# Kernel tuning notes

Measured on AMD Instinct MI355X. Metric: run time of the kernel, lower is better.

The kernel has to match this reference:

```python
import jax, jax.numpy as jnp
import numpy as np

S, B, D = 2048, 2, 1024
H, DH = 16, 64
DFF = 4096
E, K = 4, 2
SCALE = 1.0 / (DH ** 0.5)


def _ln(x, g, b, eps):
    m = jnp.mean(x, axis=-1, keepdims=True)
    v = jnp.mean((x - m) ** 2, axis=-1, keepdims=True)
    return (x - m) * jax.lax.rsqrt(v + eps) * g + b


def setup_inputs() -> dict:
    key = jax.random.key(0)
    ks = jax.random.split(key, 12)
    s = lambda k, shape, fan: jax.random.normal(k, shape, jnp.float32) * (fan ** -0.5)
    return {
        "hidden_states": jax.random.normal(ks[0], (S, B, D), jnp.float32),
        "ln_in_g": jnp.ones((D,), jnp.float32), "ln_in_b": jnp.zeros((D,), jnp.float32),
        "Wq": s(ks[1], (D, H * DH), D),
        "Wkv": s(ks[2], (D, 2 * H * DH), D),
        "Wo": s(ks[3], (H * DH, D), H * DH),
        "ln_attn_g": jnp.ones((D,), jnp.float32), "ln_attn_b": jnp.zeros((D,), jnp.float32),
        "ln_post_g": jnp.ones((D,), jnp.float32), "ln_post_b": jnp.zeros((D,), jnp.float32),
        "Wg": s(ks[4], (D, E), D),
        "W1": s(ks[5], (E, D, DFF), D), "b1": jnp.zeros((E, DFF), jnp.float32),
        "W2": s(ks[6], (E, DFF, D), DFF), "b2": jnp.zeros((E, D), jnp.float32),
    }


def reference(hidden_states, ln_in_g, ln_in_b, Wq, Wkv, Wo, ln_attn_g, ln_attn_b,
              ln_post_g, ln_post_b, Wg, W1, b1, W2, b2):
    # --- input layernorm (eps=1e-6) ---
    h = _ln(hidden_states, ln_in_g, ln_in_b, 1e-6)  # [S,B,D]

    # --- MultiHeadAttn2 (post-lnorm, no mask, no mems) ---
    q = (h @ Wq).reshape(S, B, H, DH)
    k, v = jnp.split((h @ Wkv).reshape(S, B, H, 2 * DH), 2, axis=-1)
    score = jnp.einsum('ibnd,jbnd->ijbn', q, k) * SCALE      # [S,S,B,H]
    prob = jax.nn.softmax(score, axis=1)
    attn_vec = jnp.einsum('ijbn,jbnd->ibnd', prob, v).reshape(S, B, H * DH)
    attn_out = attn_vec @ Wo
    attention_output = _ln(h + attn_out, ln_attn_g, ln_attn_b, 1e-5)

    # --- residual + post-attention layernorm (eps=1e-6) ---
    layernorm_input = hidden_states + attention_output
    x = _ln(layernorm_input, ln_post_g, ln_post_b, 1e-6)

    # --- top-k MoE (E=4, k=2, no token dropping) ---
    xt = x.reshape(-1, D)                                     # [T,D]
    probs = jax.nn.softmax(xt @ Wg, axis=-1)                  # [T,E]
    topv, topi = jax.lax.top_k(probs, K)                      # [T,K]
    gates = topv / jnp.sum(topv, axis=-1, keepdims=True)
    cw = jnp.zeros_like(probs)
    for kk in range(K):  # small fixed K
        cw = cw + gates[:, kk:kk + 1] * jax.nn.one_hot(topi[:, kk], E, dtype=probs.dtype)
    hmid = jax.nn.gelu(jnp.einsum('td,edf->tef', xt, W1) + b1, approximate=False)
    y = jnp.einsum('tef,efd->ted', hmid, W2) + b2             # [T,E,D]
    moe_out = jnp.einsum('te,ted->td', cw, y).reshape(S, B, D)

    # load-balancing aux loss: E * sum(mean_probs * top1_fraction)
    me = jnp.mean(probs, axis=0)
    ce = jnp.mean(jax.nn.one_hot(topi[:, 0], E, dtype=probs.dtype), axis=0)
    moe_loss = E * jnp.sum(me * ce)

    output = layernorm_input + moe_out
    return output, moe_loss
```

## Files before the change

### kernel.cpp

```cpp
#include <hip/hip_runtime.h>
#include <cmath>

#define S_   2048
#define B_   2
#define D_   1024
#define H_   16
#define DH_  64
#define DFF_ 4096
#define E_   4
#define T_   4096
#define SCALE_ 0.125f

typedef __attribute__((ext_vector_type(8))) short short8;
typedef __attribute__((ext_vector_type(4))) float f32x4;
typedef __attribute__((ext_vector_type(4))) unsigned short u16x4;
typedef __attribute__((ext_vector_type(4))) unsigned int u32x4;

static __device__ __forceinline__ unsigned short f2bf(float f) {
  union { float f; unsigned int u; } v; v.f = f;
  unsigned int r = v.u + 0x7FFFu + ((v.u >> 16) & 1u);
  return (unsigned short)(r >> 16);
}

static __device__ __forceinline__ float bf2f(unsigned short u) {
  union { unsigned int u; float f; } v; v.u = (unsigned int)u << 16;
  return v.f;
}

static __device__ __forceinline__ f32x4 mfma16(short8 a, short8 b, f32x4 c) {
  return __builtin_amdgcn_mfma_f32_16x16x32_bf16(a, b, c, 0, 0, 0);
}

static __device__ __forceinline__ void gll16(const unsigned short* g, unsigned short* l) {
  __builtin_amdgcn_global_load_lds(
      (const __attribute__((address_space(1))) void*)g,
      (__attribute__((address_space(3))) void*)l, 16, 0, 0);
}

static __device__ __forceinline__ float gelu_f(float vv) {
  float u = 0.7978845608f * (vv + 0.044715f * vv * vv * vv);
  u = fminf(fmaxf(u, -9.0f), 9.0f);
  float e2 = __expf(2.0f * u);
  return vv * e2 * (1.0f / (e2 + 1.0f));
}

__global__ void transpose_cvt(const float* __restrict__ in, unsigned short* __restrict__ out,
                              int R, int C) {
  __shared__ float t[64][33];
  size_t boff = (size_t)blockIdx.z * R * C;
  in += boff; out += boff;
  int c0 = blockIdx.x * 32, r0 = blockIdx.y * 64;
  for (int i = threadIdx.y; i < 64; i += 8)
    t[i][threadIdx.x] = in[(size_t)(r0 + i) * C + c0 + threadIdx.x];
  __syncthreads();
  for (int i = threadIdx.y; i < 32; i += 8) {
    float v0 = t[2 * threadIdx.x][i], v1 = t[2 * threadIdx.x + 1][i];
    unsigned int pk = (unsigned int)f2bf(v0) | ((unsigned int)f2bf(v1) << 16);
    *(unsigned int*)(&out[(size_t)(c0 + i) * R + r0 + 2 * threadIdx.x]) = pk;
  }
}

__global__ void transpose_cvt_split(const float* __restrict__ in,
    unsigned short* __restrict__ outh, unsigned short* __restrict__ outl, int R, int C) {
  __shared__ float t[64][33];
  int c0 = blockIdx.x * 32, r0 = blockIdx.y * 64;
  for (int i = threadIdx.y; i < 64; i += 8)
    t[i][threadIdx.x] = in[(size_t)(r0 + i) * C + c0 + threadIdx.x];
  __syncthreads();
  for (int i = threadIdx.y; i < 32; i += 8) {
    float v0 = t[2 * threadIdx.x][i], v1 = t[2 * threadIdx.x + 1][i];
    unsigned short h0 = f2bf(v0), h1 = f2bf(v1);
    unsigned int hp = (unsigned int)h0 | ((unsigned int)h1 << 16);
    unsigned int lp = (unsigned int)f2bf(v0 - bf2f(h0)) |
                      ((unsigned int)f2bf(v1 - bf2f(h1)) << 16);
    size_t o = (size_t)(c0 + i) * R + r0 + 2 * threadIdx.x;
    *(unsigned int*)(&outh[o]) = hp;
    *(unsigned int*)(&outl[o]) = lp;
  }
}

__global__ __launch_bounds__(256) void v_transpose(
    const unsigned short* __restrict__ kvh, const unsigned short* __restrict__ kvl,
    unsigned short* __restrict__ vTh, unsigned short* __restrict__ vTl) {
  __shared__ unsigned short th[64][72], tl[64][72];
  int j0 = blockIdx.x * 64;
  int bh = blockIdx.y;
  int b = bh & 1, n = bh >> 1;
  int tid = threadIdx.x;
  int jr = tid >> 3, dc = (tid & 7) * 8;
  for (int it = 0; it < 2; ++it) {
    int jj = it * 32 + jr;
    size_t src = ((size_t)((j0 + jj) * 2 + b)) * 2048 + n * 128 + 64 + dc;
    *(short8*)(&th[jj][dc]) = *(const short8*)(kvh + src);
    *(short8*)(&tl[jj][dc]) = *(const short8*)(kvl + src);
  }
  __syncthreads();
  int dr = tid >> 3, jc = (tid & 7) * 8;
  for (int it = 0; it < 2; ++it) {
    int d = it * 32 + dr;
    short8 oh, ol;
    for (int u = 0; u < 8; ++u) { oh[u] = th[jc + u][d]; ol[u] = tl[jc + u][d]; }
    size_t dst = ((size_t)((b * 16 + n) * 64 + d)) * 2048 + j0 + jc;
    *(short8*)(vTh + dst) = oh;
    *(short8*)(vTl + dst) = ol;
  }
}

static __device__ __forceinline__ void block_reduce2(float& s, float& s2, float* sh) {
  __syncthreads();
  for (int off = 32; off; off >>= 1) { s += __shfl_down(s, off); s2 += __shfl_down(s2, off); }
  int w = threadIdx.x >> 6;
  if ((threadIdx.x & 63) == 0) { sh[w * 2] = s; sh[w * 2 + 1] = s2; }
  __syncthreads();
  s = sh[0] + sh[2] + sh[4] + sh[6];
  s2 = sh[1] + sh[3] + sh[5] + sh[7];
}

__global__ __launch_bounds__(256) void ln_in_kernel(const float* __restrict__ hid,
    const float* __restrict__ g, const float* __restrict__ b,
    float* __restrict__ h, unsigned short* __restrict__ hbh, unsigned short* __restrict__ hbl) {
  __shared__ float sh[8];
  int t = blockIdx.x, tid = threadIdx.x;
  size_t ro = (size_t)t * D_;
  f32x4 v = ((const f32x4*)(hid + ro))[tid];
  float s = v[0] + v[1] + v[2] + v[3];
  float s2 = v[0]*v[0] + v[1]*v[1] + v[2]*v[2] + v[3]*v[3];
  block_reduce2(s, s2, sh);
  float mean = s * (1.0f / D_);
  float var = s2 * (1.0f / D_) - mean * mean;
  float rstd = rsqrtf(var + 1e-6f);
  f32x4 gv = ((const f32x4*)g)[tid], bv = ((const f32x4*)b)[tid];
  f32x4 y; u16x4 yh, yl;
  for (int c = 0; c < 4; ++c) {
    float z = (v[c] - mean) * rstd * gv[c] + bv[c];
    y[c] = z; yh[c] = f2bf(z); yl[c] = f2bf(z - bf2f(yh[c]));
  }
  ((f32x4*)(h + ro))[tid] = y;
  ((u16x4*)(hbh + ro))[tid] = yh;
  ((u16x4*)(hbl + ro))[tid] = yl;
}

__global__ __launch_bounds__(256) void ln_fused_kernel(
    const float* __restrict__ hid, const float* __restrict__ h, const float* __restrict__ ao,
    const float* __restrict__ ga, const float* __restrict__ ba,
    const float* __restrict__ gp, const float* __restrict__ bp,
    float* __restrict__ out, float* __restrict__ x, unsigned short* __restrict__ xb) {
  __shared__ float sh[8];
  int t = blockIdx.x, tid = threadIdx.x;
  size_t ro = (size_t)t * D_;
  f32x4 hv = ((const f32x4*)(h + ro))[tid];
  f32x4 av = ((const f32x4*)(ao + ro))[tid];
  f32x4 a = hv + av;
  float s = a[0] + a[1] + a[2] + a[3];
  float s2 = a[0]*a[0] + a[1]*a[1] + a[2]*a[2] + a[3]*a[3];
  block_reduce2(s, s2, sh);
  float mean = s * (1.0f / D_);
  float var = s2 * (1.0f / D_) - mean * mean;
  float rstd = rsqrtf(var + 1e-5f);
  f32x4 lg = ((const f32x4*)ga)[tid], lb = ((const f32x4*)ba)[tid];
  f32x4 hidv = ((const f32x4*)(hid + ro))[tid];
  f32x4 li;
  for (int c = 0; c < 4; ++c) li[c] = hidv[c] + (a[c] - mean) * rstd * lg[c] + lb[c];
  ((f32x4*)(out + ro))[tid] = li;
  float s3 = li[0] + li[1] + li[2] + li[3];
  float s4 = li[0]*li[0] + li[1]*li[1] + li[2]*li[2] + li[3]*li[3];
  block_reduce2(s3, s4, sh);
  float mean2 = s3 * (1.0f / D_);
  float var2 = s4 * (1.0f / D_) - mean2 * mean2;
  float rstd2 = rsqrtf(var2 + 1e-6f);
  f32x4 g2 = ((const f32x4*)gp)[tid], b2v = ((const f32x4*)bp)[tid];
  f32x4 xv; u16x4 xbv;
  for (int c = 0; c < 4; ++c) { float z = (li[c] - mean2) * rstd2 * g2[c] + b2v[c]; xv[c] = z; xbv[c] = f2bf(z); }
  ((f32x4*)(x + ro))[tid] = xv;
  ((u16x4*)(xb + ro))[tid] = xbv;
}

__global__ __launch_bounds__(256) void qkv_gemm(
    const unsigned short* __restrict__ Ah, const unsigned short* __restrict__ Al,
    const unsigned short* __restrict__ WqTh, const unsigned short* __restrict__ WqTl,
    const unsigned short* __restrict__ WkvTh, const unsigned short* __restrict__ WkvTl,
    unsigned short* __restrict__ qh, unsigned short* __restrict__ ql,
    unsigned short* __restrict__ kvh, unsigned short* __restrict__ kvl) {
  const int K = 1024;
  int m0 = blockIdx.y * 128, n0g = blockIdx.x * 128;
  const unsigned short *Bh, *Bl;
  unsigned short *Ch, *Cl;
  int NC, n0;
  float cscale;
  if (n0g < 1024) { Bh = WqTh; Bl = WqTl; Ch = qh; Cl = ql; NC = 1024; n0 = n0g; cscale = SCALE_; }
  else { Bh = WkvTh; Bl = WkvTl; Ch = kvh; Cl = kvl; NC = 2048; n0 = n0g - 1024; cscale = 1.0f; }
  __shared__ unsigned short pool2[32768];
  unsigned short* buf[2] = { pool2, pool2 + 16384 };
  int tid = threadIdx.x;
  int lane = tid & 63, w = tid >> 6;
  int quad = lane >> 4, l15 = lane & 15;
  int wm = (w >> 1) * 64, wn = (w & 1) * 64;
  f32x4 acc[4][4];
  for (int i = 0; i < 4; ++i) for (int j = 0; j < 4; ++j) acc[i][j] = 0;
  int rs0 = w * 32 + (lane >> 2), rs1 = rs0 + 16;
  int sw = ((lane & 3) ^ ((lane >> 3) & 3)) * 8;
  const unsigned short* gah0 = Ah + (size_t)(m0 + rs0) * K + sw;
  const unsigned short* gah1 = Ah + (size_t)(m0 + rs1) * K + sw;
  const unsigned short* gal0 = Al + (size_t)(m0 + rs0) * K + sw;
  const unsigned short* gal1 = Al + (size_t)(m0 + rs1) * K + sw;
  const unsigned short* gbh0 = Bh + (size_t)(n0 + rs0) * K + sw;
  const unsigned short* gbh1 = Bh + (size_t)(n0 + rs1) * K + sw;
  const unsigned short* gbl0 = Bl + (size_t)(n0 + rs0) * K + sw;
  const unsigned short* gbl1 = Bl + (size_t)(n0 + rs1) * K + sw;
  int so0 = (w * 2 + 0) * 512, so1 = (w * 2 + 1) * 512;
  int sq = (l15 >> 1) & 3;
  auto stage = [&](unsigned short* bb, int k) {
    gll16(gah0 + k, bb + so0);         gll16(gah1 + k, bb + so1);
    gll16(gal0 + k, bb + 4096 + so0);  gll16(gal1 + k, bb + 4096 + so1);
    gll16(gbh0 + k, bb + 8192 + so0);  gll16(gbh1 + k, bb + 8192 + so1);
    gll16(gbl0 + k, bb + 12288 + so0); gll16(gbl1 + k, bb + 12288 + so1);
  };
  auto compute = [&](const unsigned short* bb) {
    short8 afh[4], afl[4], bfh[4], bfl[4];
    for (int i = 0; i < 4; ++i) {
      int o = (wm + i * 16 + l15) * 32 + ((quad ^ sq) * 8);
      afh[i] = *(const short8*)(&bb[o]);
      afl[i] = *(const short8*)(&bb[4096 + o]);
    }
    for (int j = 0; j < 4; ++j) {
      int o = (wn + j * 16 + l15) * 32 + ((quad ^ sq) * 8);
      bfh[j] = *(const short8*)(&bb[8192 + o]);
      bfl[j] = *(const short8*)(&bb[12288 + o]);
    }
    for (int i = 0; i < 4; ++i)
      for (int j = 0; j < 4; ++j) {
        f32x4 a = acc[i][j];
        a = mfma16(afh[i], bfl[j], a);
        a = mfma16(afl[i], bfh[j], a);
        a = mfma16(afh[i], bfh[j], a);
        acc[i][j] = a;
      }
  };
  stage(buf[0], 0);
  __syncthreads();
  for (int k0 = 0; k0 < K; k0 += 64) {
    stage(buf[1], k0 + 32);
    compute(buf[0]);
    __syncthreads();
    if (k0 + 64 < K) stage(buf[0], k0 + 64);
    compute(buf[1]);
    __syncthreads();
  }
  unsigned short* eph = &pool2[w * 1152];
  unsigned short* epl = &pool2[4608 + w * 1152];
  int row16 = lane >> 3, chunk = lane & 7;
  for (int i = 0; i < 4; ++i) {
    for (int j = 0; j < 4; ++j) {
      f32x4 a = acc[i][j];
      int lo = j * 16 + l15;
      for (int r = 0; r < 4; ++r) {
        float av = a[r] * cscale;
        unsigned short hb = f2bf(av);
        eph[(quad * 4 + r) * 72 + lo] = hb;
        epl[(quad * 4 + r) * 72 + lo] = f2bf(av - bf2f(hb));
      }
    }
    for (int it = 0; it < 2; ++it) {
      int rr = it * 8 + row16;
      size_t go = (size_t)(m0 + wm + i * 16 + rr) * NC + n0 + wn + chunk * 8;
      *(u32x4*)(&Ch[go]) = *(const u32x4*)(&eph[rr * 72 + chunk * 8]);
      *(u32x4*)(&Cl[go]) = *(const u32x4*)(&epl[rr * 72 + chunk * 8]);
    }
    __syncthreads();
  }
}

template<int MT>
__global__ __launch_bounds__(256) void gemm3f(
    const unsigned short* __restrict__ Ah, const unsigned short* __restrict__ Al,
    const unsigned short* __restrict__ Bh, const unsigned short* __restrict__ Bl,
    float* __restrict__ Cf, int N, int K) {
  int m0 = blockIdx.y * MT, n0 = blockIdx.x * 128;
  __shared__ unsigned short pool3[MT * 64 + 8192];
  unsigned short* Ash = pool3;
  unsigned short* Asl = pool3 + MT * 32;
  unsigned short* Bsh = pool3 + MT * 64;
  unsigned short* Bsl = pool3 + MT * 64 + 4096;
  int tid = threadIdx.x;
  int lane = tid & 63, w = tid >> 6;
  int quad = lane >> 4, l15 = lane & 15;
  int wm = (w >> 1) * (MT / 2), wn = (w & 1) * 64;
  constexpr int MI = MT / 32;
  f32x4 acc[MI][4];
  for (int i = 0; i < MI; ++i) for (int j = 0; j < 4; ++j) acc[i][j] = 0;
  constexpr int AI = MT / 64;
  int cofs = (lane & 3) * 8;
  const unsigned short* gah[AI]; const unsigned short* gal[AI];
  unsigned short *lAh[AI], *lAl[AI];
  for (int is = 0; is < AI; ++is) {
    int rs = w * (MT / 4) + is * 16 + (lane >> 2);
    gah[is] = Ah + (size_t)(m0 + rs) * K + cofs;
    gal[is] = Al + (size_t)(m0 + rs) * K + cofs;
    lAh[is] = &Ash[(w * AI + is) * 512];
    lAl[is] = &Asl[(w * AI + is) * 512];
  }
  int rsB0 = w * 32 + (lane >> 2), rsB1 = rsB0 + 16;
  const unsigned short* gbh0 = Bh + (size_t)(n0 + rsB0) * K + cofs;
  const unsigned short* gbh1 = Bh + (size_t)(n0 + rsB1) * K + cofs;
  const unsigned short* gbl0 = Bl + (size_t)(n0 + rsB0) * K + cofs;
  const unsigned short* gbl1 = Bl + (size_t)(n0 + rsB1) * K + cofs;
  unsigned short* lB0 = &Bsh[(w * 2 + 0) * 512];
  unsigned short* lB1 = &Bsh[(w * 2 + 1) * 512];
  unsigned short* lBl0 = &Bsl[(w * 2 + 0) * 512];
  unsigned short* lBl1 = &Bsl[(w * 2 + 1) * 512];
  for (int k0 = 0; k0 < K; k0 += 32) {
    __syncthreads();
    for (int is = 0; is < AI; ++is) { gll16(gah[is] + k0, lAh[is]); gll16(gal[is] + k0, lAl[is]); }
    gll16(gbh0 + k0, lB0); gll16(gbh1 + k0, lB1);
    gll16(gbl0 + k0, lBl0); gll16(gbl1 + k0, lBl1);
    __syncthreads();
    short8 afh[MI], afl[MI], bfh[4], bfl[4];
    for (int i = 0; i < MI; ++i) {
      int o = (wm + i * 16 + l15) * 32 + quad * 8;
      afh[i] = *(const short8*)(&Ash[o]);
      afl[i] = *(const short8*)(&Asl[o]);
    }
    for (int j = 0; j < 4; ++j) {
      int o = (wn + j * 16 + l15) * 32 + quad * 8;
      bfh[j] = *(const short8*)(&Bsh[o]);
      bfl[j] = *(const short8*)(&Bsl[o]);
    }
    for (int i = 0; i < MI; ++i)
      for (int j = 0; j < 4; ++j) {
        f32x4 a = acc[i][j];
        a = mfma16(afh[i], bfl[j], a);
        a = mfma16(afl[i], bfh[j], a);
        a = mfma16(afh[i], bfh[j], a);
        acc[i][j] = a;
      }
  }
  __syncthreads();
  float* epf = (float*)(pool3 + w * 2176);
  for (int i = 0; i < MI; ++i) {
    for (int j = 0; j < 4; ++j) {
      f32x4 a = acc[i][j];
      for (int r = 0; r < 4; ++r) epf[(quad * 4 + r) * 68 + j * 16 + l15] = a[r];
    }
    for (int it = 0; it < 4; ++it) {
      int rr = (lane >> 4) + it * 4;
      int ch = lane & 15;
      *(f32x4*)(&Cf[(size_t)(m0 + wm + i * 16 + rr) * N + n0 + wn + ch * 4]) =
          *(const f32x4*)(&epf[rr * 68 + ch * 4]);
    }
    __syncthreads();
  }
}

__global__ __launch_bounds__(256) void moe_up(
    const unsigned short* __restrict__ A, const unsigned short* __restrict__ W1T,
    unsigned short* __restrict__ hmid, int N, int K,
    const int* __restrict__ cnt, const int* __restrict__ offs,
    const int* __restrict__ list, const float* __restrict__ b1) {
  int e = blockIdx.y >> 5, mt = blockIdx.y & 31;
  int M = cnt[e];
  int m0 = mt * 128, n0 = blockIdx.x * 128;
  if (M == 0 || m0 >= M) return;
  const unsigned short* Bt = W1T + (size_t)e * DFF_ * D_;
  const int* liste = list + e * T_;
  const float* bias = b1 + (size_t)e * DFF_;
  size_t obase = (size_t)offs[e];
  __shared__ unsigned short pool[16384];
  unsigned short* As0 = pool;
  unsigned short* Bs0 = pool + 4096;
  unsigned short* As1 = pool + 8192;
  unsigned short* Bs1 = pool + 12288;
  int tid = threadIdx.x;
  int lane = tid & 63, w = tid >> 6;
  int quad = lane >> 4, l15 = lane & 15;
  int wm = (w >> 1) * 64, wn = (w & 1) * 64;
  f32x4 acc[4][4];
  for (int i = 0; i < 4; ++i) for (int j = 0; j < 4; ++j) acc[i][j] = 0;
  int rs0 = w * 32 + (lane >> 2), rs1 = rs0 + 16;
  int sw = ((lane & 3) ^ ((lane >> 3) & 3)) * 8;
  const unsigned short* ga0 = A + (size_t)liste[min(m0 + rs0, M - 1)] * K + sw;
  const unsigned short* ga1 = A + (size_t)liste[min(m0 + rs1, M - 1)] * K + sw;
  const unsigned short* gb0 = Bt + (size_t)(n0 + rs0) * K + sw;
  const unsigned short* gb1 = Bt + (size_t)(n0 + rs1) * K + sw;
  int so0 = (w * 2 + 0) * 512, so1 = (w * 2 + 1) * 512;
  int sq = (l15 >> 1) & 3;
  auto stage = [&](unsigned short* Ab, unsigned short* Bb, int k) {
    gll16(ga0 + k, Ab + so0); gll16(ga1 + k, Ab + so1);
    gll16(gb0 + k, Bb + so0); gll16(gb1 + k, Bb + so1);
  };
  auto compute = [&](const unsigned short* Ab, const unsigned short* Bb) {
    short8 af[4], bfr[4];
    for (int i = 0; i < 4; ++i)
      af[i] = *(const short8*)(&Ab[(wm + i * 16 + l15) * 32 + (quad ^ sq) * 8]);
    for (int j = 0; j < 4; ++j)
      bfr[j] = *(const short8*)(&Bb[(wn + j * 16 + l15) * 32 + (quad ^ sq) * 8]);
    for (int i = 0; i < 4; ++i)
      for (int j = 0; j < 4; ++j)
        acc[i][j] = mfma16(af[i], bfr[j], acc[i][j]);
  };
  stage(As0, Bs0, 0);
  __syncthreads();
  for (int k0 = 0; k0 < K; k0 += 64) {
    stage(As1, Bs1, k0 + 32);
    compute(As0, Bs0);
    __syncthreads();
    if (k0 + 64 < K) stage(As0, Bs0, k0 + 64);
    compute(As1, Bs1);
    __syncthreads();
  }
  unsigned short* ep = &pool[w * 1152];
  int row16 = lane >> 3, chunk = lane & 7;
  for (int i = 0; i < 4; ++i) {
    for (int j = 0; j < 4; ++j) {
      f32x4 a = acc[i][j];
      int colg = n0 + wn + j * 16 + l15;
      float bv = bias[colg];
      for (int r = 0; r < 4; ++r)
        ep[(quad * 4 + r) * 72 + j * 16 + l15] = f2bf(gelu_f(a[r] + bv));
    }
    for (int it = 0; it < 2; ++it) {
      int rr = it * 8 + row16;
      int rowg = m0 + wm + i * 16 + rr;
      if (rowg < M)
        *(u32x4*)(&hmid[(obase + rowg) * DFF_ + n0 + wn + chunk * 8]) =
            *(const u32x4*)(&ep[rr * 72 + chunk * 8]);
    }
  }
}

__global__ __launch_bounds__(256) void moe_down(
    const unsigned short* __restrict__ hmid, const unsigned short* __restrict__ W2T,
    int N, int K,
    const int* __restrict__ cnt, const int* __restrict__ offs,
    const int* __restrict__ list, const float* __restrict__ gatev,
    const float* __restrict__ b2, float* __restrict__ accum) {
  int e = blockIdx.y >> 5, mt = blockIdx.y & 31;
  int M = cnt[e];
  int m0 = mt * 128, n0 = blockIdx.x * 128;
  if (M == 0 || m0 >= M) return;
  const unsigned short* A = hmid + (size_t)offs[e] * DFF_;
  const unsigned short* Bt = W2T + (size_t)e * D_ * DFF_;
  const int* liste = list + e * T_;
  const float* gv = gatev + e * T_;
  const float* bias = b2 + (size_t)e * D_;
  __shared__ unsigned short pool[16384];
  unsigned short* As0 = pool;
  unsigned short* Bs0 = pool + 4096;
  unsigned short* As1 = pool + 8192;
  unsigned short* Bs1 = pool + 12288;
  int tid = threadIdx.x;
  int lane = tid & 63, w = tid >> 6;
  int quad = lane >> 4, l15 = lane & 15;
  int wm = (w >> 1) * 64, wn = (w & 1) * 64;
  f32x4 acc[4][4];
  for (int i = 0; i < 4; ++i) for (int j = 0; j < 4; ++j) acc[i][j] = 0;
  int rs0 = w * 32 + (lane >> 2), rs1 = rs0 + 16;
  int sw = ((lane & 3) ^ ((lane >> 3) & 3)) * 8;
  const unsigned short* ga0 = A + (size_t)min(m0 + rs0, M - 1) * K + sw;
  const unsigned short* ga1 = A + (size_t)min(m0 + rs1, M - 1) * K + sw;
  const unsigned short* gb0 = Bt + (size_t)(n0 + rs0) * K + sw;
  const unsigned short* gb1 = Bt + (size_t)(n0 + rs1) * K + sw;
  int so0 = (w * 2 + 0) * 512, so1 = (w * 2 + 1) * 512;
  int sq = (l15 >> 1) & 3;
  auto stage = [&](unsigned short* Ab, unsigned short* Bb, int k) {
    gll16(ga0 + k, Ab + so0); gll16(ga1 + k, Ab + so1);
    gll16(gb0 + k, Bb + so0); gll16(gb1 + k, Bb + so1);
  };
  auto compute = [&](const unsigned short* Ab, const unsigned short* Bb) {
    short8 af[4], bfr[4];
    for (int i = 0; i < 4; ++i)
      af[i] = *(const short8*)(&Ab[(wm + i * 16 + l15) * 32 + (quad ^ sq) * 8]);
    for (int j = 0; j < 4; ++j)
      bfr[j] = *(const short8*)(&Bb[(wn + j * 16 + l15) * 32 + (quad ^ sq) * 8]);
    for (int i = 0; i < 4; ++i)
      for (int j = 0; j < 4; ++j)
        acc[i][j] = mfma16(af[i], bfr[j], acc[i][j]);
  };
  stage(As0, Bs0, 0);
  __syncthreads();
  for (int k0 = 0; k0 < K; k0 += 64) {
    stage(As1, Bs1, k0 + 32);
    compute(As0, Bs0);
    __syncthreads();
    if (k0 + 64 < K) stage(As0, Bs0, k0 + 64);
    compute(As1, Bs1);
    __syncthreads();
  }
  for (int i = 0; i < 4; ++i) for (int j = 0; j < 4; ++j) {
    int row = m0 + wm + i * 16 + quad * 4;
    int col = n0 + wn + j * 16 + l15;
    f32x4 a = acc[i][j];
    float bv = bias[col];
    for (int r = 0; r < 4; ++r) if (row + r < M) {
      int tt = liste[row + r];
      float gg = gv[row + r];
      atomicAdd(&accum[(size_t)tt * D_ + col], gg * (a[r] + bv));
    }
  }
}

__global__ __launch_bounds__(256, 2) void attn_kernel(
    const unsigned short* __restrict__ qh, const unsigned short* __restrict__ ql,
    const unsigned short* __restrict__ kvh, const unsigned short* __restrict__ kvl,
    const unsigned short* __restrict__ vTh, const unsigned short* __restrict__ vTl,
    unsigned short* __restrict__ avh, unsigned short* __restrict__ avl) {
  int bh = blockIdx.x;
  int itile = blockIdx.y;
  int b = bh & 1, n = bh >> 1;
  __shared__ unsigned short Kh[2][4096], Kl[2][4096], Vh[2][4096], Vl[2][4096];
  __shared__ unsigned short Ps[4][1152];
  int tid = threadIdx.x;
  int w = tid >> 6, lane = tid & 63, quad = lane >> 4, l15 = lane & 15;
  int i_base = itile * 64 + w * 16;
  short8 qfh[2], qfl[2];
  {
    size_t qo = ((size_t)((i_base + l15) * B_ + b)) * 1024 + n * 64;
    qfh[0] = *(const short8*)(qh + qo + quad * 8);
    qfh[1] = *(const short8*)(qh + qo + 32 + quad * 8);
    qfl[0] = *(const short8*)(ql + qo + quad * 8);
    qfl[1] = *(const short8*)(ql + qo + 32 + quad * 8);
  }
  float m_i[4], lp[4];
  f32x4 o[4];
  for (int r = 0; r < 4; ++r) { m_i[r] = -1e30f; lp[r] = 0.0f; }
  for (int d = 0; d < 4; ++d) o[d] = 0;
  int jk = tid >> 3;
  int ck = (tid & 7) ^ (jk & 7);
  size_t kS = ((size_t)(jk * 2 + b)) * 2048 + (size_t)n * 128 + ck * 8;
  size_t vS = ((size_t)((b * 16 + n) * 64 + jk)) * 2048 + ck * 8;
  int ldst = tid * 8;
  unsigned short* psw = &Ps[w][0];
  gll16(kvh + kS, &Kh[0][ldst]);           gll16(kvh + kS + 131072, &Kh[0][2048 + ldst]);
  gll16(kvl + kS, &Kl[0][ldst]);           gll16(kvl + kS + 131072, &Kl[0][2048 + ldst]);
  gll16(vTh + vS, &Vh[0][ldst]);           gll16(vTh + vS + 65536, &Vh[0][2048 + ldst]);
  gll16(vTl + vS, &Vl[0][ldst]);           gll16(vTl + vS + 65536, &Vl[0][2048 + ldst]);
  __syncthreads();
  for (int jt = 0; jt < 32; ++jt) {
    int cur = jt & 1;
    if (jt < 31) {
      int nb = cur ^ 1;
      size_t ks2 = kS + (size_t)(jt + 1) * 262144;
      size_t vs2 = vS + (size_t)(jt + 1) * 64;
      gll16(kvh + ks2, &Kh[nb][ldst]);     gll16(kvh + ks2 + 131072, &Kh[nb][2048 + ldst]);
      gll16(kvl + ks2, &Kl[nb][ldst]);     gll16(kvl + ks2 + 131072, &Kl[nb][2048 + ldst]);
      gll16(vTh + vs2, &Vh[nb][ldst]);     gll16(vTh + vs2 + 65536, &Vh[nb][2048 + ldst]);
      gll16(vTl + vs2, &Vl[nb][ldst]);     gll16(vTl + vs2 + 65536, &Vl[nb][2048 + ldst]);
    }
    f32x4 sac[4];
    __builtin_amdgcn_s_setprio(1);
    for (int t4 = 0; t4 < 4; ++t4) {
      int j = t4 * 16 + l15;
      int base = j * 64;
      int c0 = (quad ^ (j & 7)) << 3;
      int c1 = ((quad | 4) ^ (j & 7)) << 3;
      short8 kh0 = *(const short8*)(&Kh[cur][base + c0]);
      short8 kh1 = *(const short8*)(&Kh[cur][base + c1]);
      short8 kl0 = *(const short8*)(&Kl[cur][base + c0]);
      short8 kl1 = *(const short8*)(&Kl[cur][base + c1]);
      f32x4 a = 0;
      a = mfma16(qfh[0], kl0, a);
      a = mfma16(qfh[1], kl1, a);
      a = mfma16(qfl[0], kh0, a);
      a = mfma16(qfl[1], kh1, a);
      a = mfma16(qfh[0], kh0, a);
      a = mfma16(qfh[1], kh1, a);
      sac[t4] = a;
    }
    __builtin_amdgcn_s_setprio(0);
    float m1[4];
    for (int r = 0; r < 4; ++r) {
      float v = fmaxf(fmaxf(sac[0][r], sac[1][r]), fmaxf(sac[2][r], sac[3][r]));
      for (int off = 1; off < 16; off <<= 1) v = fmaxf(v, __shfl_xor(v, off, 16));
      m1[r] = v;
    }
    float p[4][4];
    bool ok = (m1[0] <= m_i[0] + 8.f) && (m1[1] <= m_i[1] + 8.f) &&
              (m1[2] <= m_i[2] + 8.f) && (m1[3] <= m_i[3] + 8.f);
    if (__all(ok)) {
      for (int r = 0; r < 4; ++r) {
        float rs = 0.f;
        for (int t4 = 0; t4 < 4; ++t4) {
          float pp = __expf(sac[t4][r] - m_i[r]);
          p[t4][r] = pp; rs += pp;
        }
        lp[r] += rs;
      }
    } else {
      float alpha[4];
      for (int r = 0; r < 4; ++r) {
        float mnew = fmaxf(m_i[r], m1[r]);
        alpha[r] = __expf(m_i[r] - mnew);
        m_i[r] = mnew;
        float rs = 0.f;
        for (int t4 = 0; t4 < 4; ++t4) {
          float pp = __expf(sac[t4][r] - mnew);
          p[t4][r] = pp; rs += pp;
        }
        lp[r] = lp[r] * alpha[r] + rs;
      }
      for (int d = 0; d < 4; ++d) for (int r = 0; r < 4; ++r) o[d][r] *= alpha[r];
    }
    for (int t4 = 0; t4 < 4; ++t4) for (int r = 0; r < 4; ++r)
      psw[(quad * 4 + r) * 72 + t4 * 16 + l15] = f2bf(p[t4][r]);
    __builtin_amdgcn_s_setprio(1);
    for (int dblk = 0; dblk < 4; ++dblk) {
      f32x4 a = o[dblk];
      int d = dblk * 16 + l15;
      int vb = d * 64;
      for (int ks = 0; ks < 2; ++ks) {
        short8 pfh = *(const short8*)(&psw[l15 * 72 + ks * 32 + quad * 8]);
        int ch = ((ks * 4 + quad) ^ (d & 7)) << 3;
        short8 vfh = *(const short8*)(&Vh[cur][vb + ch]);
        short8 vfl = *(const short8*)(&Vl[cur][vb + ch]);
        a = mfma16(pfh, vfl, a);
        a = mfma16(pfh, vfh, a);
      }
      o[dblk] = a;
    }
    __builtin_amdgcn_s_setprio(0);
    __syncthreads();
  }
  float l_i[4];
  for (int r = 0; r < 4; ++r) {
    float v = lp[r];
    for (int off = 1; off < 16; off <<= 1) v += __shfl_xor(v, off, 16);
    l_i[r] = v;
  }
  {
    int row16 = lane >> 3, chunk = lane & 7;
    for (int d = 0; d < 4; ++d) for (int r = 0; r < 4; ++r) {
      float val = o[d][r] / l_i[r];
      psw[(quad * 4 + r) * 72 + d * 16 + l15] = f2bf(val);
    }
    for (int it = 0; it < 2; ++it) {
      int rr = it * 8 + row16;
      size_t go = ((size_t)((i_base + rr) * B_ + b)) * 1024 + n * 64 + chunk * 8;
      *(u32x4*)(&avh[go]) = *(const u32x4*)(&psw[rr * 72 + chunk * 8]);
    }
    __syncthreads();
    for (int d = 0; d < 4; ++d) for (int r = 0; r < 4; ++r) {
      float val = o[d][r] / l_i[r];
      unsigned short hb = f2bf(val);
      psw[(quad * 4 + r) * 72 + d * 16 + l15] = f2bf(val - bf2f(hb));
    }
    for (int it = 0; it < 2; ++it) {
      int rr = it * 8 + row16;
      size_t go = ((size_t)((i_base + rr) * B_ + b)) * 1024 + n * 64 + chunk * 8;
      *(u32x4*)(&avl[go]) = *(const u32x4*)(&psw[rr * 72 + chunk * 8]);
    }
  }
}

__global__ __launch_bounds__(256) void gate_kernel(const float* __restrict__ x,
    const float* __restrict__ Wg, int* __restrict__ cnt,
    float* __restrict__ me_sum, float* __restrict__ ce_sum,
    int* __restrict__ list, float* __restrict__ gatev) {
  __shared__ float sl[64][4];
  int w = threadIdx.x >> 6, lane = threadIdx.x & 63;
  int tbase = blockIdx.x * 64;
  for (int k = 0; k < 16; ++k) {
    int t = tbase + w * 16 + k;
    f32x4 acc = 0;
    const float* xr = x + (size_t)t * D_;
    for (int j = 0; j < 16; ++j) {
      int d = j * 64 + lane;
      float xd = xr[d];
      f32x4 wg = ((const f32x4*)Wg)[d];
      acc += xd * wg;
    }
    for (int c = 0; c < 4; ++c) {
      float vv = acc[c];
      for (int off = 32; off; off >>= 1) vv += __shfl_down(vv, off);
      if (lane == 0) sl[w * 16 + k][c] = vv;
    }
  }
  __syncthreads();
  if (w == 0) {
    int t = tbase + lane;
    float p[4];
    float mx = fmaxf(fmaxf(sl[lane][0], sl[lane][1]), fmaxf(sl[lane][2], sl[lane][3]));
    float sum = 0.f;
    for (int e = 0; e < 4; ++e) { p[e] = expf(sl[lane][e] - mx); sum += p[e]; }
    float inv = 1.0f / sum;
    for (int e = 0; e < 4; ++e) p[e] *= inv;
    int i0 = 0;
    for (int e = 1; e < 4; ++e) if (p[e] > p[i0]) i0 = e;
    int i1 = (i0 == 0) ? 1 : 0;
    for (int e = 0; e < 4; ++e) if (e != i0 && p[e] > p[i1]) i1 = e;
    float g0 = p[i0] / (p[i0] + p[i1]);
    float g1 = p[i1] / (p[i0] + p[i1]);
    for (int e = 0; e < 4; ++e) {
      float vv = p[e];
      for (int off = 32; off; off >>= 1) vv += __shfl_down(vv, off);
      if (lane == 0) atomicAdd(&me_sum[e], vv);
    }
    unsigned long long lbm = (1ull << lane) - 1;
    for (int e = 0; e < 4; ++e) {
      unsigned long long m0 = __ballot(i0 == e);
      int tot = __popcll(m0);
      int base = 0;
      if (lane == e && tot > 0) {
        base = atomicAdd(&cnt[e], tot);
        atomicAdd(&ce_sum[e], (float)tot);
      }
      base = __shfl(base, e);
      if (i0 == e) {
        int pos = base + __popcll(m0 & lbm);
        list[e * T_ + pos] = t;
        gatev[e * T_ + pos] = g0;
      }
      unsigned long long m1 = __ballot(i1 == e);
      int tot1 = __popcll(m1);
      int base1 = 0;
      if (lane == e && tot1 > 0) base1 = atomicAdd(&cnt[e], tot1);
      base1 = __shfl(base1, e);
      if (i1 == e) {
        int pos = base1 + __popcll(m1 & lbm);
        list[e * T_ + pos] = t;
        gatev[e * T_ + pos] = g1;
      }
    }
  }
}

__global__ void loss_offs_kernel(const float* __restrict__ me, const float* __restrict__ ce,
                                 const int* __restrict__ cnt, int* __restrict__ offs,
                                 float* __restrict__ out) {
  if (threadIdx.x == 0) {
    float l = 0.f;
    for (int e = 0; e < E_; ++e) l += (me[e] * (1.0f / T_)) * (ce[e] * (1.0f / T_));
    out[0] = (float)E_ * l;
    int o = 0;
    for (int e = 0; e < E_; ++e) { offs[e] = o; o += cnt[e]; }
  }
}

extern "C" void kernel_launch(void* const* d_in, const int* in_sizes, int n_in,
                              void* d_out, int out_size, void* d_ws, size_t ws_size,
                              hipStream_t stream) {
  const float* hid       = (const float*)d_in[0];
  const float* ln_in_g   = (const float*)d_in[1];
  const float* ln_in_b   = (const float*)d_in[2];
  const float* Wq        = (const float*)d_in[3];
  const float* Wkv       = (const float*)d_in[4];
  const float* Wo        = (const float*)d_in[5];
  const float* ln_attn_g = (const float*)d_in[6];
  const float* ln_attn_b = (const float*)d_in[7];
  const float* ln_post_g = (const float*)d_in[8];
  const float* ln_post_b = (const float*)d_in[9];
  const float* Wg        = (const float*)d_in[10];
  const float* W1        = (const float*)d_in[11];
  const float* b1        = (const float*)d_in[12];
  const float* W2        = (const float*)d_in[13];
  const float* b2        = (const float*)d_in[14];
  float* out = (float*)d_out;

  char* p = (char*)d_ws;
  size_t off = 0;
  auto alloc = [&](size_t bytes) -> void* {
    void* r = p + off; off += (bytes + 255) & ~(size_t)255; return r;
  };
  float* h        = (float*)alloc((size_t)T_ * D_ * 4);
  float* x        = (float*)alloc((size_t)T_ * D_ * 4);
  unsigned short* hmid_all = (unsigned short*)h;
  unsigned short* qh = (unsigned short*)alloc((size_t)T_ * 1024 * 2);
  unsigned short* ql = (unsigned short*)alloc((size_t)T_ * 1024 * 2);
  float* attn_out = (float*)qh;
  unsigned short* hbh = (unsigned short*)alloc((size_t)T_ * D_ * 2);
  unsigned short* hbl = (unsigned short*)alloc((size_t)T_ * D_ * 2);
  unsigned short* vTh = hbh;
  unsigned short* vTl = hbl;
  unsigned short* xb  = (unsigned short*)alloc((size_t)T_ * D_ * 2);
  unsigned short* kvh = (unsigned short*)alloc((size_t)T_ * 2048 * 2);
  unsigned short* kvl = (unsigned short*)alloc((size_t)T_ * 2048 * 2);
  unsigned short* W1T = kvh;
  unsigned short* avh = (unsigned short*)alloc((size_t)T_ * 1024 * 2);
  unsigned short* avl = (unsigned short*)alloc((size_t)T_ * 1024 * 2);
  unsigned short* W2T = avh;
  unsigned short* WqTh  = (unsigned short*)alloc((size_t)1024 * 1024 * 2);
  unsigned short* WqTl  = (unsigned short*)alloc((size_t)1024 * 1024 * 2);
  unsigned short* WkvTh = (unsigned short*)alloc((size_t)2048 * 1024 * 2);
  unsigned short* WkvTl = (unsigned short*)alloc((size_t)2048 * 1024 * 2);
  unsigned short* WoTh  = (unsigned short*)alloc((size_t)1024 * 1024 * 2);
  unsigned short* WoTl  = (unsigned short*)alloc((size_t)1024 * 1024 * 2);
  void* ghdr = alloc(256);
  int* cnt = (int*)ghdr;
  float* me_sum = (float*)ghdr + 4;
  float* ce_sum = (float*)ghdr + 8;
  int* offs = (int*)ghdr + 12;
  int* list = (int*)alloc((size_t)E_ * T_ * 4);
  float* gatev = (float*)alloc((size_t)E_ * T_ * 4);

  hipMemsetAsync(ghdr, 0, 64, stream);

  dim3 tb(32, 8);
  transpose_cvt_split<<<dim3(32, 16), tb, 0, stream>>>(Wq, WqTh, WqTl, 1024, 1024);
  transpose_cvt_split<<<dim3(64, 16), tb, 0, stream>>>(Wkv, WkvTh, WkvTl, 1024, 2048);
  transpose_cvt_split<<<dim3(32, 16), tb, 0, stream>>>(Wo, WoTh, WoTl, 1024, 1024);

  ln_in_kernel<<<T_, 256, 0, stream>>>(hid, ln_in_g, ln_in_b, h, hbh, hbl);

  qkv_gemm<<<dim3(24, 32), 256, 0, stream>>>(hbh, hbl, WqTh, WqTl, WkvTh, WkvTl,
      qh, ql, kvh, kvl);

  v_transpose<<<dim3(32, 32), 256, 0, stream>>>(kvh, kvl, vTh, vTl);

  attn_kernel<<<dim3(32, 32), 256, 0, stream>>>(qh, ql, kvh, kvl, vTh, vTl, avh, avl);

  gemm3f<64><<<dim3(8, 64), 256, 0, stream>>>(avh, avl, WoTh, WoTl, attn_out, 1024, 1024);

  ln_fused_kernel<<<T_, 256, 0, stream>>>(hid, h, attn_out, ln_attn_g, ln_attn_b,
      ln_post_g, ln_post_b, out, x, xb);

  gate_kernel<<<T_ / 64, 256, 0, stream>>>(x, Wg, cnt, me_sum, ce_sum, list, gatev);
  loss_offs_kernel<<<1, 64, 0, stream>>>(me_sum, ce_sum, cnt, offs, out + (size_t)T_ * D_);

  transpose_cvt<<<dim3(128, 16, 4), tb, 0, stream>>>(W1, W1T, 1024, 4096);
  transpose_cvt<<<dim3(32, 64, 4), tb, 0, stream>>>(W2, W2T, 4096, 1024);

  moe_up<<<dim3(32, 128), 256, 0, stream>>>(xb, W1T, hmid_all, DFF_, 1024,
      cnt, offs, list, b1);
  moe_down<<<dim3(8, 128), 256, 0, stream>>>(hmid_all, W2T, D_, DFF_,
      cnt, offs, list, gatev, b2, out);
}
```

Measured before the change: 826.0 us.

## Double MoE GEMM k-tile to 64 with 8-way swizzle and reorder down grid

Both MoE expert GEMMs now stage 64-wide K slices into shared memory instead of 32, with a new XOR swizzle over 8 chunks. This halves the barrier count and the per-iteration overhead. moe_down's grid is also transposed so that consecutive blocks walk the M tiles of one expert for a fixed N tile, which changes L2 reuse of the weight columns. The cost is double the LDS per block (64KB), which may lower occupancy.

```diff
diff --git a/kernel.cpp b/kernel.cpp
--- a/kernel.cpp
+++ b/kernel.cpp
@@ -364,46 +364,53 @@
   const int* liste = list + e * T_;
   const float* bias = b1 + (size_t)e * DFF_;
   size_t obase = (size_t)offs[e];
-  __shared__ unsigned short pool[16384];
+  __shared__ unsigned short pool[32768];
   unsigned short* As0 = pool;
-  unsigned short* Bs0 = pool + 4096;
-  unsigned short* As1 = pool + 8192;
-  unsigned short* Bs1 = pool + 12288;
+  unsigned short* Bs0 = pool + 8192;
+  unsigned short* As1 = pool + 16384;
+  unsigned short* Bs1 = pool + 24576;
   int tid = threadIdx.x;
   int lane = tid & 63, w = tid >> 6;
   int quad = lane >> 4, l15 = lane & 15;
   int wm = (w >> 1) * 64, wn = (w & 1) * 64;
+  int r7 = l15 & 7;
   f32x4 acc[4][4];
   for (int i = 0; i < 4; ++i) for (int j = 0; j < 4; ++j) acc[i][j] = 0;
-  int rs0 = w * 32 + (lane >> 2), rs1 = rs0 + 16;
-  int sw = ((lane & 3) ^ ((lane >> 3) & 3)) * 8;
-  const unsigned short* ga0 = A + (size_t)liste[min(m0 + rs0, M - 1)] * K + sw;
-  const unsigned short* ga1 = A + (size_t)liste[min(m0 + rs1, M - 1)] * K + sw;
-  const unsigned short* gb0 = Bt + (size_t)(n0 + rs0) * K + sw;
-  const unsigned short* gb1 = Bt + (size_t)(n0 + rs1) * K + sw;
-  int so0 = (w * 2 + 0) * 512, so1 = (w * 2 + 1) * 512;
-  int sq = (l15 >> 1) & 3;
+  int srow = lane >> 3;
+  int swc = ((lane & 7) ^ srow) * 8;
+  const unsigned short* gA[4]; const unsigned short* gB[4];
+  for (int i = 0; i < 4; ++i) {
+    int ra = m0 + w * 32 + i * 8 + srow;
+    gA[i] = A + (size_t)liste[min(ra, M - 1)] * K + swc;
+    gB[i] = Bt + (size_t)(n0 + w * 32 + i * 8 + srow) * K + swc;
+  }
+  int lbase = w * 2048;
   auto stage = [&](unsigned short* Ab, unsigned short* Bb, int k) {
-    gll16(ga0 + k, Ab + so0); gll16(ga1 + k, Ab + so1);
-    gll16(gb0 + k, Bb + so0); gll16(gb1 + k, Bb + so1);
+    for (int i = 0; i < 4; ++i) {
+      gll16(gA[i] + k, Ab + lbase + i * 512);
+      gll16(gB[i] + k, Bb + lbase + i * 512);
+    }
   };
   auto compute = [&](const unsigned short* Ab, const unsigned short* Bb) {
-    short8 af[4], bfr[4];
-    for (int i = 0; i < 4; ++i)
-      af[i] = *(const short8*)(&Ab[(wm + i * 16 + l15) * 32 + (quad ^ sq) * 8]);
-    for (int j = 0; j < 4; ++j)
-      bfr[j] = *(const short8*)(&Bb[(wn + j * 16 + l15) * 32 + (quad ^ sq) * 8]);
-    for (int i = 0; i < 4; ++i)
+    for (int h = 0; h < 2; ++h) {
+      int ch = ((h * 4 + quad) ^ r7) * 8;
+      short8 af[4], bfr[4];
+      for (int i = 0; i < 4; ++i)
+        af[i] = *(const short8*)(&Ab[(wm + i * 16 + l15) * 64 + ch]);
       for (int j = 0; j < 4; ++j)
-        acc[i][j] = mfma16(af[i], bfr[j], acc[i][j]);
+        bfr[j] = *(const short8*)(&Bb[(wn + j * 16 + l15) * 64 + ch]);
+      for (int i = 0; i < 4; ++i)
+        for (int j = 0; j < 4; ++j)
+          acc[i][j] = mfma16(af[i], bfr[j], acc[i][j]);
+    }
   };
   stage(As0, Bs0, 0);
   __syncthreads();
-  for (int k0 = 0; k0 < K; k0 += 64) {
-    stage(As1, Bs1, k0 + 32);
+  for (int k0 = 0; k0 < K; k0 += 128) {
+    stage(As1, Bs1, k0 + 64);
     compute(As0, Bs0);
     __syncthreads();
-    if (k0 + 64 < K) stage(As0, Bs0, k0 + 64);
+    if (k0 + 128 < K) stage(As0, Bs0, k0 + 128);
     compute(As1, Bs1);
     __syncthreads();
   }
@@ -433,55 +440,62 @@
     const int* __restrict__ cnt, const int* __restrict__ offs,
     const int* __restrict__ list, const float* __restrict__ gatev,
     const float* __restrict__ b2, float* __restrict__ accum) {
-  int e = blockIdx.y >> 5, mt = blockIdx.y & 31;
+  int e = blockIdx.x >> 5, mt = blockIdx.x & 31;
   int M = cnt[e];
-  int m0 = mt * 128, n0 = blockIdx.x * 128;
+  int m0 = mt * 128, n0 = blockIdx.y * 128;
   if (M == 0 || m0 >= M) return;
   const unsigned short* A = hmid + (size_t)offs[e] * DFF_;
   const unsigned short* Bt = W2T + (size_t)e * D_ * DFF_;
   const int* liste = list + e * T_;
   const float* gv = gatev + e * T_;
   const float* bias = b2 + (size_t)e * D_;
-  __shared__ unsigned short pool[16384];
+  __shared__ unsigned short pool[32768];
   unsigned short* As0 = pool;
-  unsigned short* Bs0 = pool + 4096;
-  unsigned short* As1 = pool + 8192;
-  unsigned short* Bs1 = pool + 12288;
+  unsigned short* Bs0 = pool + 8192;
+  unsigned short* As1 = pool + 16384;
+  unsigned short* Bs1 = pool + 24576;
   int tid = threadIdx.x;
   int lane = tid & 63, w = tid >> 6;
   int quad = lane >> 4, l15 = lane & 15;
   int wm = (w >> 1) * 64, wn = (w & 1) * 64;
+  int r7 = l15 & 7;
   f32x4 acc[4][4];
   for (int i = 0; i < 4; ++i) for (int j = 0; j < 4; ++j) acc[i][j] = 0;
-  int rs0 = w * 32 + (lane >> 2), rs1 = rs0 + 16;
-  int sw = ((lane & 3) ^ ((lane >> 3) & 3)) * 8;
-  const unsigned short* ga0 = A + (size_t)min(m0 + rs0, M - 1) * K + sw;
-  const unsigned short* ga1 = A + (size_t)min(m0 + rs1, M - 1) * K + sw;
-  const unsigned short* gb0 = Bt + (size_t)(n0 + rs0) * K + sw;
-  const unsigned short* gb1 = Bt + (size_t)(n0 + rs1) * K + sw;
-  int so0 = (w * 2 + 0) * 512, so1 = (w * 2 + 1) * 512;
-  int sq = (l15 >> 1) & 3;
+  int srow = lane >> 3;
+  int swc = ((lane & 7) ^ srow) * 8;
+  const unsigned short* gA[4]; const unsigned short* gB[4];
+  for (int i = 0; i < 4; ++i) {
+    int ra = m0 + w * 32 + i * 8 + srow;
+    gA[i] = A + (size_t)min(ra, M - 1) * K + swc;
+    gB[i] = Bt + (size_t)(n0 + w * 32 + i * 8 + srow) * K + swc;
+  }
+  int lbase = w * 2048;
   auto stage = [&](unsigned short* Ab, unsigned short* Bb, int k) {
-    gll16(ga0 + k, Ab + so0); gll16(ga1 + k, Ab + so1);
-    gll16(gb0 + k, Bb + so0); gll16(gb1 + k, Bb + so1);
+    for (int i = 0; i < 4; ++i) {
+      gll16(gA[i] + k, Ab + lbase + i * 512);
+      gll16(gB[i] + k, Bb + lbase + i * 512);
+    }
   };
   auto compute = [&](const unsigned short* Ab, const unsigned short* Bb) {
-    short8 af[4], bfr[4];
-    for (int i = 0; i < 4; ++i)
-      af[i] = *(const short8*)(&Ab[(wm + i * 16 + l15) * 32 + (quad ^ sq) * 8]);
-    for (int j = 0; j < 4; ++j)
-      bfr[j] = *(const short8*)(&Bb[(wn + j * 16 + l15) * 32 + (quad ^ sq) * 8]);
-    for (int i = 0; i < 4; ++i)
+    for (int h = 0; h < 2; ++h) {
+      int ch = ((h * 4 + quad) ^ r7) * 8;
+      short8 af[4], bfr[4];
+      for (int i = 0; i < 4; ++i)
+        af[i] = *(const short8*)(&Ab[(wm + i * 16 + l15) * 64 + ch]);
       for (int j = 0; j < 4; ++j)
-        acc[i][j] = mfma16(af[i], bfr[j], acc[i][j]);
+        bfr[j] = *(const short8*)(&Bb[(wn + j * 16 + l15) * 64 + ch]);
+      for (int i = 0; i < 4; ++i)
+        for (int j = 0; j < 4; ++j)
+          acc[i][j] = mfma16(af[i], bfr[j], acc[i][j]);
+    }
   };
   stage(As0, Bs0, 0);
   __syncthreads();
-  for (int k0 = 0; k0 < K; k0 += 64) {
-    stage(As1, Bs1, k0 + 32);
+  for (int k0 = 0; k0 < K; k0 += 128) {
+    stage(As1, Bs1, k0 + 64);
     compute(As0, Bs0);
     __syncthreads();
-    if (k0 + 64 < K) stage(As0, Bs0, k0 + 64);
+    if (k0 + 128 < K) stage(As0, Bs0, k0 + 128);
     compute(As1, Bs1);
     __syncthreads();
   }
@@ -819,6 +833,6 @@
 
   moe_up<<<dim3(32, 128), 256, 0, stream>>>(xb, W1T, hmid_all, DFF_, 1024,
       cnt, offs, list, b1);
-  moe_down<<<dim3(8, 128), 256, 0, stream>>>(hmid_all, W2T, D_, DFF_,
+  moe_down<<<dim3(E_ * 32, 8), 256, 0, stream>>>(hmid_all, W2T, D_, DFF_,
       cnt, offs, list, gatev, b2, out);
 }
```

Result: no change. 842.0 us (+1.9%).

## Triple-buffer MoE GEMM K-loop with one barrier per step and partial vmcnt waits

Applied to the files above, without the earlier changes.

Both MoE GEMM kernels now use a three-stage LDS ring instead of double buffering. Each 32-wide K step issues a single barrier, and the wait on outstanding global-to-LDS loads is partial (vmcnt(4)), so one stage stays in flight while the current one is computed. The aim is to hide global load latency and halve the barriers per K step. The cost is 48KB of LDS per block instead of 32KB, which may cut occupancy, and the explicit vmcnt accounting must match the loads each stage actually issues.

```diff
diff --git a/kernel.cpp b/kernel.cpp
--- a/kernel.cpp
+++ b/kernel.cpp
@@ -364,11 +364,9 @@
   const int* liste = list + e * T_;
   const float* bias = b1 + (size_t)e * DFF_;
   size_t obase = (size_t)offs[e];
-  __shared__ unsigned short pool[16384];
-  unsigned short* As0 = pool;
-  unsigned short* Bs0 = pool + 4096;
-  unsigned short* As1 = pool + 8192;
-  unsigned short* Bs1 = pool + 12288;
+  __shared__ unsigned short pool[24576];
+  unsigned short* bufA[3] = { pool,         pool + 8192,  pool + 16384 };
+  unsigned short* bufB[3] = { pool + 4096,  pool + 12288, pool + 20480 };
   int tid = threadIdx.x;
   int lane = tid & 63, w = tid >> 6;
   int quad = lane >> 4, l15 = lane & 15;
@@ -397,16 +395,23 @@
       for (int j = 0; j < 4; ++j)
         acc[i][j] = mfma16(af[i], bfr[j], acc[i][j]);
   };
-  stage(As0, Bs0, 0);
-  __syncthreads();
-  for (int k0 = 0; k0 < K; k0 += 64) {
-    stage(As1, Bs1, k0 + 32);
-    compute(As0, Bs0);
-    __syncthreads();
-    if (k0 + 64 < K) stage(As0, Bs0, k0 + 64);
-    compute(As1, Bs1);
-    __syncthreads();
-  }
+  stage(bufA[0], bufB[0], 0);
+  stage(bufA[1], bufB[1], 32);
+  unsigned short *a0 = bufA[0], *b0 = bufB[0];
+  unsigned short *a1 = bufA[1], *b1v = bufB[1];
+  unsigned short *a2 = bufA[2], *b2v = bufB[2];
+  for (int k0 = 0; k0 < K; k0 += 32) {
+    if (k0 + 32 < K) asm volatile("s_waitcnt vmcnt(4)" ::: "memory");
+    else             asm volatile("s_waitcnt vmcnt(0)" ::: "memory");
+    __builtin_amdgcn_s_barrier();
+    asm volatile("" ::: "memory");
+    if (k0 + 64 < K) stage(a2, b2v, k0 + 64);
+    compute(a0, b0);
+    unsigned short* t;
+    t = a0; a0 = a1; a1 = a2; a2 = t;
+    t = b0; b0 = b1v; b1v = b2v; b2v = t;
+  }
+  __syncthreads();
   unsigned short* ep = &pool[w * 1152];
   int row16 = lane >> 3, chunk = lane & 7;
   for (int i = 0; i < 4; ++i) {
@@ -442,11 +447,9 @@
   const int* liste = list + e * T_;
   const float* gv = gatev + e * T_;
   const float* bias = b2 + (size_t)e * D_;
-  __shared__ unsigned short pool[16384];
-  unsigned short* As0 = pool;
-  unsigned short* Bs0 = pool + 4096;
-  unsigned short* As1 = pool + 8192;
-  unsigned short* Bs1 = pool + 12288;
+  __shared__ unsigned short pool[24576];
+  unsigned short* bufA[3] = { pool,         pool + 8192,  pool + 16384 };
+  unsigned short* bufB[3] = { pool + 4096,  pool + 12288, pool + 20480 };
   int tid = threadIdx.x;
   int lane = tid & 63, w = tid >> 6;
   int quad = lane >> 4, l15 = lane & 15;
@@ -475,16 +478,23 @@
       for (int j = 0; j < 4; ++j)
         acc[i][j] = mfma16(af[i], bfr[j], acc[i][j]);
   };
-  stage(As0, Bs0, 0);
-  __syncthreads();
-  for (int k0 = 0; k0 < K; k0 += 64) {
-    stage(As1, Bs1, k0 + 32);
-    compute(As0, Bs0);
-    __syncthreads();
-    if (k0 + 64 < K) stage(As0, Bs0, k0 + 64);
-    compute(As1, Bs1);
-    __syncthreads();
-  }
+  stage(bufA[0], bufB[0], 0);
+  stage(bufA[1], bufB[1], 32);
+  unsigned short *a0 = bufA[0], *b0 = bufB[0];
+  unsigned short *a1 = bufA[1], *b1v = bufB[1];
+  unsigned short *a2 = bufA[2], *b2v = bufB[2];
+  for (int k0 = 0; k0 < K; k0 += 32) {
+    if (k0 + 32 < K) asm volatile("s_waitcnt vmcnt(4)" ::: "memory");
+    else             asm volatile("s_waitcnt vmcnt(0)" ::: "memory");
+    __builtin_amdgcn_s_barrier();
+    asm volatile("" ::: "memory");
+    if (k0 + 64 < K) stage(a2, b2v, k0 + 64);
+    compute(a0, b0);
+    unsigned short* t;
+    t = a0; a0 = a1; a1 = a2; a2 = t;
+    t = b0; b0 = b1v; b1v = b2v; b2v = t;
+  }
+  __syncthreads();
   for (int i = 0; i < 4; ++i) for (int j = 0; j < 4; ++j) {
     int row = m0 + wm + i * 16 + quad * 4;
     int col = n0 + wn + j * 16 + l15;
```

Result: no change. 815.4 us (-1.3%).
